# Kernel tuning notes

Measured on AMD Instinct MI355X. Metric: run time of the kernel, lower is better.

## Reference

```python
import jax, jax.numpy as jnp
import numpy as np

N = 50000      # nodes
F_IN = 128     # in_features
F_OUT = 128    # out_features
E = 800000     # edges (avg degree 16)


def setup_inputs() -> dict:
    key = jax.random.key(0)
    k = jax.random.split(key, 6)
    x = jax.random.normal(k[0], (N, F_IN), dtype=jnp.float32)
    h0 = jax.random.normal(k[1], (N, F_IN), dtype=jnp.float32)
    edge_row = jax.random.randint(k[2], (E,), 0, N, dtype=jnp.int32)
    edge_col = jax.random.randint(k[3], (E,), 0, N, dtype=jnp.int32)
    # normalized-Laplacian-like positive weights
    edge_val = jax.random.uniform(k[4], (E,), dtype=jnp.float32)
    stdv = 1.0 / np.sqrt(F_OUT)
    weight = jax.random.uniform(k[5], (F_IN, F_OUT), dtype=jnp.float32,
                                minval=-stdv, maxval=stdv)
    return {
        "input": x,
        "h0": h0,
        "edge_row": edge_row,
        "edge_col": edge_col,
        "edge_val": edge_val,
        "weight": weight,
        "lamda": jnp.float32(0.5),
        "alpha": jnp.float32(0.1),
        "l": 4,  # layer index (python int)
    }


def reference(input, h0, edge_row, edge_col, edge_val, weight, lamda, alpha, l):
    # theta = log(lamda / l + 1)
    theta = jnp.log(lamda / l + 1.0)
    # hi = spmm(G, input): gather source features, scale by edge value, scatter-add to rows
    msgs = edge_val[:, None] * input[edge_col]              # [E, F]
    hi = jax.ops.segment_sum(msgs, edge_row, num_segments=N)  # [N, F]
    # variant=False: support == r == (1-alpha)*hi + alpha*h0
    support = (1.0 - alpha) * hi + alpha * h0
    out = theta * (support @ weight) + (1.0 - theta) * support
    # residual=True
    out = out + input
    return out
```

## Files before the change

### kernel.cpp

```cpp
#include <hip/hip_runtime.h>
#include <math.h>

#define NF 128
#define SCAN_B 1024


__global__ __launch_bounds__(256) void zero_kernel(int* __restrict__ p, int n) {
    int i = blockIdx.x * 256 + threadIdx.x;
    if (i < n) p[i] = 0;
}

__global__ __launch_bounds__(256) void hist_kernel(
    const int* __restrict__ erow, int* __restrict__ cnt, int E_) {
    int e = blockIdx.x * 256 + threadIdx.x;
    if (e < E_) atomicAdd(&cnt[erow[e]], 1);
}

__global__ __launch_bounds__(SCAN_B) void scanA_kernel(
    const int* __restrict__ cnt, int* __restrict__ bsum, int N_) {
    __shared__ int buf[SCAN_B];
    int t = threadIdx.x;
    int i = blockIdx.x * SCAN_B + t;
    buf[t] = (i < N_) ? cnt[i] : 0;
    __syncthreads();
    for (int d = SCAN_B / 2; d > 0; d >>= 1) {
        if (t < d) buf[t] += buf[t + d];
        __syncthreads();
    }
    if (t == 0) bsum[blockIdx.x] = buf[0];
}

__global__ __launch_bounds__(64) void scanB_kernel(
    const int* __restrict__ bsum, int* __restrict__ bpre,
    int* __restrict__ off_total, int nb) {
    int t = threadIdx.x;
    int v0 = (t < nb) ? bsum[t] : 0;
    int v = v0;
    for (int d = 1; d < 64; d <<= 1) {
        int u = __shfl_up(v, d, 64);
        if (t >= d) v += u;
    }
    if (t < nb) bpre[t] = v - v0;
    if (t == nb - 1) *off_total = v;
}

__global__ __launch_bounds__(SCAN_B) void scanC_kernel(
    const int* __restrict__ cnt, const int* __restrict__ bpre,
    int* __restrict__ off, int* __restrict__ pos, int N_) {
    __shared__ int buf[SCAN_B];
    int t = threadIdx.x;
    int i = blockIdx.x * SCAN_B + t;
    int v = (i < N_) ? cnt[i] : 0;
    buf[t] = v;
    __syncthreads();
    for (int d = 1; d < SCAN_B; d <<= 1) {
        int add = (t >= d) ? buf[t - d] : 0;
        __syncthreads();
        buf[t] += add;
        __syncthreads();
    }
    if (i < N_) {
        int o = bpre[blockIdx.x] + buf[t] - v;
        off[i] = o;
        pos[i] = o;
    }
}

__global__ __launch_bounds__(256) void fill_kernel(
    const int* __restrict__ erow, const int* __restrict__ ecol,
    const float* __restrict__ evalv, int* __restrict__ pos,
    int* __restrict__ scol, float* __restrict__ sval, int E_) {
    int e = blockIdx.x * 256 + threadIdx.x;
    if (e >= E_) return;
    int p = atomicAdd(&pos[erow[e]], 1);
    scol[p] = ecol[e];
    sval[p] = evalv[e];
}


__global__ __launch_bounds__(256) void spmm_kernel(
    const float* __restrict__ x, const float* __restrict__ h0,
    const int* __restrict__ off, const int* __restrict__ scol,
    const float* __restrict__ sval, float* __restrict__ sup,
    const float* __restrict__ alpha_p, int N_) {
    int w = (blockIdx.x * 256 + threadIdx.x) >> 6;
    if (w >= N_) return;
    int lane = threadIdx.x & 63;
    float alpha = *alpha_p;
    int s = off[w], e = off[w + 1];
    float2 acc = {0.f, 0.f};
    int i = s;
    for (; i + 3 < e; i += 4) {
        int c0 = scol[i], c1 = scol[i + 1], c2 = scol[i + 2], c3 = scol[i + 3];
        float v0 = sval[i], v1 = sval[i + 1], v2 = sval[i + 2], v3 = sval[i + 3];
        float2 a = *((const float2*)(x + (size_t)c0 * NF) + lane);
        float2 b = *((const float2*)(x + (size_t)c1 * NF) + lane);
        float2 c = *((const float2*)(x + (size_t)c2 * NF) + lane);
        float2 d = *((const float2*)(x + (size_t)c3 * NF) + lane);
        acc.x += v0 * a.x + v1 * b.x + v2 * c.x + v3 * d.x;
        acc.y += v0 * a.y + v1 * b.y + v2 * c.y + v3 * d.y;
    }
    for (; i < e; i++) {
        int c0 = scol[i];
        float v0 = sval[i];
        float2 a = *((const float2*)(x + (size_t)c0 * NF) + lane);
        acc.x += v0 * a.x;
        acc.y += v0 * a.y;
    }
    float2 h = *((const float2*)(h0 + (size_t)w * NF) + lane);
    float oma = 1.0f - alpha;
    float2 o;
    o.x = oma * acc.x + alpha * h.x;
    o.y = oma * acc.y + alpha * h.y;
    *((float2*)(sup + (size_t)w * NF) + lane) = o;
}


__global__ __launch_bounds__(256) void gemm_epilogue_kernel(
    const float* __restrict__ sup, const float* __restrict__ W,
    const float* __restrict__ inp, float* __restrict__ out,
    const float* __restrict__ lamda_p, const int* __restrict__ l_p, int n_rows) {
    __shared__ float Ws[NF * NF];
    int tid = threadIdx.x;
    for (int i = tid; i < NF * NF / 4; i += 256)
        ((float4*)Ws)[i] = ((const float4*)W)[i];
    __syncthreads();

    float theta = logf((*lamda_p) / (float)(*l_p) + 1.0f);
    float omt = 1.0f - theta;

    int m0   = blockIdx.x * 32;
    int tcol = tid & 31;
    int trow = tid >> 5;
    int n    = tcol * 4;
    int mbase = m0 + trow * 4;

    int mr[4];
#pragma unroll
    for (int r = 0; r < 4; r++) {
        int m = mbase + r;
        mr[r] = (m < n_rows) ? m : (n_rows - 1);
    }

    float acc[4][4] = {};
    for (int k = 0; k < NF; k += 4) {
        float4 srow[4];
#pragma unroll
        for (int r = 0; r < 4; r++)
            srow[r] = *(const float4*)&sup[(size_t)mr[r] * NF + k];
#pragma unroll
        for (int kk = 0; kk < 4; kk++) {
            float4 w = *(const float4*)&Ws[(k + kk) * NF + n];
#pragma unroll
            for (int r = 0; r < 4; r++) {
                float s = (&srow[r].x)[kk];
                acc[r][0] += s * w.x;
                acc[r][1] += s * w.y;
                acc[r][2] += s * w.z;
                acc[r][3] += s * w.w;
            }
        }
    }

#pragma unroll
    for (int r = 0; r < 4; r++) {
        int m = mbase + r;
        if (m >= n_rows) break;
        float4 sv = *(const float4*)&sup[(size_t)m * NF + n];
        float4 iv = *(const float4*)&inp[(size_t)m * NF + n];
        float4 o;
        o.x = theta * acc[r][0] + omt * sv.x + iv.x;
        o.y = theta * acc[r][1] + omt * sv.y + iv.y;
        o.z = theta * acc[r][2] + omt * sv.z + iv.z;
        o.w = theta * acc[r][3] + omt * sv.w + iv.w;
        *(float4*)&out[(size_t)m * NF + n] = o;
    }
}

extern "C" void kernel_launch(void* const* d_in, const int* in_sizes, int n_in,
                              void* d_out, int out_size, void* d_ws, size_t ws_size,
                              hipStream_t stream) {
    const float* x       = (const float*)d_in[0];
    const float* h0      = (const float*)d_in[1];
    const int*   erow    = (const int*)d_in[2];
    const int*   ecol    = (const int*)d_in[3];
    const float* evalv   = (const float*)d_in[4];
    const float* W       = (const float*)d_in[5];
    const float* lamda_p = (const float*)d_in[6];
    const float* alpha_p = (const float*)d_in[7];
    const int*   l_p     = (const int*)d_in[8];

    int N_ = in_sizes[0] / NF;
    int E_ = in_sizes[2];
    int nb = (N_ + SCAN_B - 1) / SCAN_B;

    char* ws = (char*)d_ws;
    size_t o = 0;
    auto alloc = [&](size_t bytes) { char* p = ws + o; o = (o + bytes + 255) & ~(size_t)255; return p; };
    float* sup  = (float*)alloc((size_t)N_ * NF * sizeof(float));
    int*   cnt  = (int*)  alloc((size_t)N_ * sizeof(int));
    int*   off  = (int*)  alloc((size_t)(N_ + 1) * sizeof(int));
    int*   pos  = (int*)  alloc((size_t)N_ * sizeof(int));
    int*   scol = (int*)  alloc((size_t)E_ * sizeof(int));
    float* sval = (float*)alloc((size_t)E_ * sizeof(float));
    int*   bsum = (int*)  alloc((size_t)nb * sizeof(int));
    int*   bpre = (int*)  alloc((size_t)nb * sizeof(int));

    float* out = (float*)d_out;

    zero_kernel<<<(N_ + 255) / 256, 256, 0, stream>>>(cnt, N_);
    hist_kernel<<<(E_ + 255) / 256, 256, 0, stream>>>(erow, cnt, E_);
    scanA_kernel<<<nb, SCAN_B, 0, stream>>>(cnt, bsum, N_);
    scanB_kernel<<<1, 64, 0, stream>>>(bsum, bpre, off + N_, nb);
    scanC_kernel<<<nb, SCAN_B, 0, stream>>>(cnt, bpre, off, pos, N_);
    fill_kernel<<<(E_ + 255) / 256, 256, 0, stream>>>(erow, ecol, evalv, pos, scol, sval, E_);

    int blocks = (N_ * 64 + 255) / 256;
    spmm_kernel<<<blocks, 256, 0, stream>>>(x, h0, off, scol, sval, sup, alpha_p, N_);

    gemm_epilogue_kernel<<<(N_ + 31) / 32, 256, 0, stream>>>(
        sup, W, x, out, lamda_p, l_p, N_);
}
```

Baseline: 311.1 us.

## Pack CSR col/val, split SpMM wave into half-warps, fuse scan stages

Packs the CSR column index and edge value into one int2 array so each edge needs a single 8-byte load. The SpMM wave is split into two 32-lane halves that process alternate edges with float4 feature loads, then combined with a cross-half shuffle. The block-prefix scan kernel is folded into the final scan kernel, and the zeroing kernel becomes a memset, saving launches. In exchange there is a shuffle reduction and half the lanes sit idle during the epilogue store.

```diff
diff --git a/kernel.cpp b/kernel.cpp
--- a/kernel.cpp
+++ b/kernel.cpp
@@ -4,11 +4,6 @@
 #define NF 128
 #define SCAN_B 1024
 
-
-__global__ __launch_bounds__(256) void zero_kernel(int* __restrict__ p, int n) {
-    int i = blockIdx.x * 256 + threadIdx.x;
-    if (i < n) p[i] = 0;
-}
 
 __global__ __launch_bounds__(256) void hist_kernel(
     const int* __restrict__ erow, int* __restrict__ cnt, int E_) {
@@ -30,25 +25,22 @@
     if (t == 0) bsum[blockIdx.x] = buf[0];
 }
 
-__global__ __launch_bounds__(64) void scanB_kernel(
-    const int* __restrict__ bsum, int* __restrict__ bpre,
-    int* __restrict__ off_total, int nb) {
+__global__ __launch_bounds__(SCAN_B) void scanC_kernel(
+    const int* __restrict__ cnt, const int* __restrict__ bsum,
+    int* __restrict__ off, int* __restrict__ pos, int N_, int nb) {
+    __shared__ int buf[SCAN_B];
+    __shared__ int bpre_sh;
     int t = threadIdx.x;
-    int v0 = (t < nb) ? bsum[t] : 0;
-    int v = v0;
-    for (int d = 1; d < 64; d <<= 1) {
-        int u = __shfl_up(v, d, 64);
-        if (t >= d) v += u;
-    }
-    if (t < nb) bpre[t] = v - v0;
-    if (t == nb - 1) *off_total = v;
-}
-
-__global__ __launch_bounds__(SCAN_B) void scanC_kernel(
-    const int* __restrict__ cnt, const int* __restrict__ bpre,
-    int* __restrict__ off, int* __restrict__ pos, int N_) {
-    __shared__ int buf[SCAN_B];
-    int t = threadIdx.x;
+    if (t < 64) {
+        int v0 = (t < nb) ? bsum[t] : 0;
+        int v = v0;
+        for (int d = 1; d < 64; d <<= 1) {
+            int u = __shfl_up(v, d, 64);
+            if (t >= d) v += u;
+        }
+        if (t == (int)blockIdx.x) bpre_sh = v - v0;
+        if (blockIdx.x == 0 && t == nb - 1) off[N_] = v;
+    }
     int i = blockIdx.x * SCAN_B + t;
     int v = (i < N_) ? cnt[i] : 0;
     buf[t] = v;
@@ -60,7 +52,7 @@
         __syncthreads();
     }
     if (i < N_) {
-        int o = bpre[blockIdx.x] + buf[t] - v;
+        int o = bpre_sh + buf[t] - v;
         off[i] = o;
         pos[i] = o;
     }
@@ -69,50 +61,65 @@
 __global__ __launch_bounds__(256) void fill_kernel(
     const int* __restrict__ erow, const int* __restrict__ ecol,
     const float* __restrict__ evalv, int* __restrict__ pos,
-    int* __restrict__ scol, float* __restrict__ sval, int E_) {
+    int2* __restrict__ epack, int E_) {
     int e = blockIdx.x * 256 + threadIdx.x;
     if (e >= E_) return;
     int p = atomicAdd(&pos[erow[e]], 1);
-    scol[p] = ecol[e];
-    sval[p] = evalv[e];
+    int2 pk;
+    pk.x = ecol[e];
+    pk.y = __float_as_int(evalv[e]);
+    epack[p] = pk;
 }
 
 
 __global__ __launch_bounds__(256) void spmm_kernel(
     const float* __restrict__ x, const float* __restrict__ h0,
-    const int* __restrict__ off, const int* __restrict__ scol,
-    const float* __restrict__ sval, float* __restrict__ sup,
-    const float* __restrict__ alpha_p, int N_) {
+    const int* __restrict__ off, const int2* __restrict__ epack,
+    float* __restrict__ sup, const float* __restrict__ alpha_p, int N_) {
     int w = (blockIdx.x * 256 + threadIdx.x) >> 6;
     if (w >= N_) return;
     int lane = threadIdx.x & 63;
-    float alpha = *alpha_p;
+    int sub  = lane & 31;
+    int half = lane >> 5;
     int s = off[w], e = off[w + 1];
-    float2 acc = {0.f, 0.f};
-    int i = s;
-    for (; i + 3 < e; i += 4) {
-        int c0 = scol[i], c1 = scol[i + 1], c2 = scol[i + 2], c3 = scol[i + 3];
-        float v0 = sval[i], v1 = sval[i + 1], v2 = sval[i + 2], v3 = sval[i + 3];
-        float2 a = *((const float2*)(x + (size_t)c0 * NF) + lane);
-        float2 b = *((const float2*)(x + (size_t)c1 * NF) + lane);
-        float2 c = *((const float2*)(x + (size_t)c2 * NF) + lane);
-        float2 d = *((const float2*)(x + (size_t)c3 * NF) + lane);
-        acc.x += v0 * a.x + v1 * b.x + v2 * c.x + v3 * d.x;
-        acc.y += v0 * a.y + v1 * b.y + v2 * c.y + v3 * d.y;
-    }
-    for (; i < e; i++) {
-        int c0 = scol[i];
-        float v0 = sval[i];
-        float2 a = *((const float2*)(x + (size_t)c0 * NF) + lane);
+    float4 acc = {0.f, 0.f, 0.f, 0.f};
+    int i = s + half;
+    for (; i + 2 < e; i += 4) {
+        int2 e0 = epack[i];
+        int2 e1 = epack[i + 2];
+        float v0 = __int_as_float(e0.y);
+        float v1 = __int_as_float(e1.y);
+        float4 a = *((const float4*)(x + (size_t)e0.x * NF) + sub);
+        float4 b = *((const float4*)(x + (size_t)e1.x * NF) + sub);
+        acc.x += v0 * a.x + v1 * b.x;
+        acc.y += v0 * a.y + v1 * b.y;
+        acc.z += v0 * a.z + v1 * b.z;
+        acc.w += v0 * a.w + v1 * b.w;
+    }
+    for (; i < e; i += 2) {
+        int2 e0 = epack[i];
+        float v0 = __int_as_float(e0.y);
+        float4 a = *((const float4*)(x + (size_t)e0.x * NF) + sub);
         acc.x += v0 * a.x;
         acc.y += v0 * a.y;
-    }
-    float2 h = *((const float2*)(h0 + (size_t)w * NF) + lane);
-    float oma = 1.0f - alpha;
-    float2 o;
-    o.x = oma * acc.x + alpha * h.x;
-    o.y = oma * acc.y + alpha * h.y;
-    *((float2*)(sup + (size_t)w * NF) + lane) = o;
+        acc.z += v0 * a.z;
+        acc.w += v0 * a.w;
+    }
+    acc.x += __shfl_xor(acc.x, 32, 64);
+    acc.y += __shfl_xor(acc.y, 32, 64);
+    acc.z += __shfl_xor(acc.z, 32, 64);
+    acc.w += __shfl_xor(acc.w, 32, 64);
+    if (half == 0) {
+        float alpha = *alpha_p;
+        float oma = 1.0f - alpha;
+        float4 h = *((const float4*)(h0 + (size_t)w * NF) + sub);
+        float4 o;
+        o.x = oma * acc.x + alpha * h.x;
+        o.y = oma * acc.y + alpha * h.y;
+        o.z = oma * acc.z + alpha * h.z;
+        o.w = oma * acc.w + alpha * h.w;
+        *((float4*)(sup + (size_t)w * NF) + sub) = o;
+    }
 }
 
 
@@ -197,26 +204,23 @@
     char* ws = (char*)d_ws;
     size_t o = 0;
     auto alloc = [&](size_t bytes) { char* p = ws + o; o = (o + bytes + 255) & ~(size_t)255; return p; };
-    float* sup  = (float*)alloc((size_t)N_ * NF * sizeof(float));
-    int*   cnt  = (int*)  alloc((size_t)N_ * sizeof(int));
-    int*   off  = (int*)  alloc((size_t)(N_ + 1) * sizeof(int));
-    int*   pos  = (int*)  alloc((size_t)N_ * sizeof(int));
-    int*   scol = (int*)  alloc((size_t)E_ * sizeof(int));
-    float* sval = (float*)alloc((size_t)E_ * sizeof(float));
-    int*   bsum = (int*)  alloc((size_t)nb * sizeof(int));
-    int*   bpre = (int*)  alloc((size_t)nb * sizeof(int));
+    float* sup   = (float*)alloc((size_t)N_ * NF * sizeof(float));
+    int*   cnt   = (int*)  alloc((size_t)N_ * sizeof(int));
+    int*   off   = (int*)  alloc((size_t)(N_ + 1) * sizeof(int));
+    int*   pos   = (int*)  alloc((size_t)N_ * sizeof(int));
+    int2*  epack = (int2*) alloc((size_t)E_ * sizeof(int2));
+    int*   bsum  = (int*)  alloc((size_t)nb * sizeof(int));
 
     float* out = (float*)d_out;
 
-    zero_kernel<<<(N_ + 255) / 256, 256, 0, stream>>>(cnt, N_);
+    hipMemsetAsync(cnt, 0, (size_t)N_ * sizeof(int), stream);
     hist_kernel<<<(E_ + 255) / 256, 256, 0, stream>>>(erow, cnt, E_);
     scanA_kernel<<<nb, SCAN_B, 0, stream>>>(cnt, bsum, N_);
-    scanB_kernel<<<1, 64, 0, stream>>>(bsum, bpre, off + N_, nb);
-    scanC_kernel<<<nb, SCAN_B, 0, stream>>>(cnt, bpre, off, pos, N_);
-    fill_kernel<<<(E_ + 255) / 256, 256, 0, stream>>>(erow, ecol, evalv, pos, scol, sval, E_);
+    scanC_kernel<<<nb, SCAN_B, 0, stream>>>(cnt, bsum, off, pos, N_, nb);
+    fill_kernel<<<(E_ + 255) / 256, 256, 0, stream>>>(erow, ecol, evalv, pos, epack, E_);
 
     int blocks = (N_ * 64 + 255) / 256;
-    spmm_kernel<<<blocks, 256, 0, stream>>>(x, h0, off, scol, sval, sup, alpha_p, N_);
+    spmm_kernel<<<blocks, 256, 0, stream>>>(x, h0, off, epack, sup, alpha_p, N_);
 
     gemm_epilogue_kernel<<<(N_ + 31) / 32, 256, 0, stream>>>(
         sup, W, x, out, lamda_p, l_p, N_);
```

Result: faster. 294.6 us (-5.3%).
